# Optimization experiments

Hardware: AMD Instinct MI355X
Metric: run time of the kernel (lower is better)

## Reference

```python
import jax, jax.numpy as jnp
import numpy as np

N = 200000
W = 255  # hidden width hard-coded in the module


def _linear_params(key, fan_in, fan_out, w_std=0.02, b_val=0.0):
    kw, _ = jax.random.split(key)
    w = jax.random.normal(kw, (fan_in, fan_out), dtype=jnp.float32) * w_std
    b = jnp.full((fan_out,), b_val, dtype=jnp.float32)
    return w, b


def setup_inputs() -> dict:
    key = jax.random.key(0)
    ks = jax.random.split(key, 20)
    inp = {
        "opacity_emb": jax.random.normal(ks[0], (N, 1), dtype=jnp.float32),
        "shs_emb": jax.random.normal(ks[1], (N, 16, 3), dtype=jnp.float32),
        "time_emb": jax.random.uniform(ks[2], (N, 1), dtype=jnp.float32),
        "semantic_feature": jax.random.normal(ks[3], (N, 128), dtype=jnp.float32),
        "point": jax.random.normal(ks[4], (N, 3), dtype=jnp.float32),
        "scales_input": jax.random.normal(ks[5], (N, 3), dtype=jnp.float32),
        "rotations_input": jax.random.normal(ks[6], (N, 4), dtype=jnp.float32),
        "dx": jax.random.normal(ks[7], (N, 3), dtype=jnp.float32),
    }
    # mask_net: ReLU -> Linear(W,W) -> ReLU -> Linear(W,1) -> sigmoid
    inp["mask_w1"], inp["mask_b1"] = _linear_params(ks[8], W, W)
    inp["mask_w2"], inp["mask_b2"] = _linear_params(ks[9], W, 1)
    # deform heads: ReLU -> Linear(W,W) -> ReLU -> Linear(W,out)
    inp["pos_w1"], inp["pos_b1"] = _linear_params(ks[10], W, W)
    inp["pos_w2"], inp["pos_b2"] = _linear_params(ks[11], W, 3)
    inp["scl_w1"], inp["scl_b1"] = _linear_params(ks[12], W, W)
    inp["scl_w2"], inp["scl_b2"] = _linear_params(ks[13], W, 3)
    inp["rot_w1"], inp["rot_b1"] = _linear_params(ks[14], W, W)
    inp["rot_w2"], inp["rot_b2"] = _linear_params(ks[15], W, 4)
    inp["shs_w1"], inp["shs_b1"] = _linear_params(ks[16], W, W)
    inp["shs_w2"], inp["shs_b2"] = _linear_params(ks[17], W, 48)
    return inp


def _head(hidden, w1, b1, w2, b2):
    # ReLU -> Linear -> ReLU -> Linear (matches nn.Sequential in the module)
    h = jax.nn.relu(hidden)
    h = jax.nn.relu(h @ w1 + b1)
    return h @ w2 + b2


def _time_pos_enc(time_emb, n):
    # vectorized version of the scalar sin/cos for-loop: uses only time_emb[0, 0]
    t = time_emb[0, 0]
    i = jnp.arange(0, 64, 2, dtype=jnp.float32)          # even indices
    freq = jnp.power(jnp.float32(10000.0), i / jnp.float32(32.0))  # 10000**(2*i/64)
    enc = jnp.stack([jnp.sin(t / freq), jnp.cos(t / freq)], axis=1).reshape(64)
    return jnp.broadcast_to(enc[None, :], (n, 64))


def reference(opacity_emb, shs_emb, time_emb, semantic_feature, point,
              scales_input, rotations_input, dx,
              mask_w1, mask_b1, mask_w2, mask_b2,
              pos_w1, pos_b1, pos_w2, pos_b2,
              scl_w1, scl_b1, scl_w2, scl_b2,
              rot_w1, rot_b1, rot_w2, rot_b2,
              shs_w1, shs_b1, shs_w2, shs_b2):
    n = shs_emb.shape[0]
    shs_flat = shs_emb.reshape(n, 48)
    tpe = _time_pos_enc(time_emb, n)                     # [N, 64]
    hidden = jnp.concatenate(
        (point, rotations_input, scales_input, opacity_emb,
         shs_flat, semantic_feature, dx, time_emb, tpe), axis=1)  # [N, 255]

    mask = jax.nn.sigmoid(_head(hidden, mask_w1, mask_b1, mask_w2, mask_b2))  # [N, 1]

    dx_out = _head(hidden, pos_w1, pos_b1, pos_w2, pos_b2)        # [N, 3]
    pts = point + dx_out * mask

    ds = _head(hidden, scl_w1, scl_b1, scl_w2, scl_b2)            # [N, 3]
    scales = scales_input + ds * mask

    dr = _head(hidden, rot_w1, rot_b1, rot_w2, rot_b2)            # [N, 4]
    rotations = rotations_input + dr * mask

    opacity = opacity_emb[:, :1]

    dshs = _head(hidden, shs_w1, shs_b1, shs_w2, shs_b2).reshape(n, 16, 3)
    shs = shs_emb + dshs * mask[:, :, None]

    return (pts, scales, rotations, opacity, shs, dx_out, dshs)
```

## Files before the change

kernel.cpp:

```cpp
#include <hip/hip_runtime.h>
#include <math.h>

typedef unsigned short u16;
typedef __attribute__((ext_vector_type(8))) short short8;
typedef __attribute__((ext_vector_type(4))) float floatx4;

__device__ __forceinline__ u16 f2bf(float f) {
    union { float f; unsigned u; } v; v.f = f;
    unsigned r = v.u + 0x7fffu + ((v.u >> 16) & 1u);
    return (u16)(r >> 16);
}

struct WPtrs {
    const float* w1[5];
    const float* w2[5];
};

typedef const __attribute__((address_space(1))) unsigned GUA;
typedef __attribute__((address_space(3))) unsigned LUA;

__device__ __forceinline__ void stage32(const u16* gbase, u16* lbase, int wave, int lane) {
    const char* g = (const char*)gbase;
    char* l = (char*)lbase;
#pragma unroll
    for (int i = 0; i < 4; ++i) {
        int off = (wave * 4 + i) * 1024;
        __builtin_amdgcn_global_load_lds((GUA*)(g + off + lane * 16), (LUA*)(l + off), 16, 0, 0);
    }
}

__global__ void prep_weights(WPtrs p, const float* __restrict__ te,
                             u16* __restrict__ W1t, u16* __restrict__ W2t,
                             float* __restrict__ W2f, u16* __restrict__ enc)
{
    const int bid = blockIdx.x;
    const int tid = threadIdx.x;
    if (bid < 80) {
        __shared__ float tile[64 * 65];
        int h = bid / 16, t = bid % 16;
        int k0 = (t / 4) * 64, n0 = (t % 4) * 64;
        int nn = tid & 63, g = tid >> 6;
        const float* w1 = p.w1[h];
#pragma unroll
        for (int rep = 0; rep < 16; ++rep) {
            int kl = g * 16 + rep;
            int k = k0 + kl, nidx = n0 + nn;
            float v = (k < 255 && nidx < 255) ? w1[k * 255 + nidx] : 0.0f;
            tile[kl * 65 + nn] = v;
        }
        __syncthreads();
#pragma unroll
        for (int i = 0; i < 2; ++i) {
            int c = tid * 2 + i;
            int nl = c >> 3, kcl = c & 7;
            int n = n0 + nl;
            int kcg = (k0 >> 3) + kcl;
            short8 sv;
#pragma unroll
            for (int j = 0; j < 8; ++j)
                sv[j] = (short)f2bf(tile[(kcl * 8 + j) * 65 + nl]);
            *(short8*)(W1t + h * 65536 + n * 256 + (((kcg ^ (n & 31))) << 3)) = sv;
        }
    } else if (bid < 192) {
        int row = bid - 80;
        int h, roff, od;
        if (row < 16)      { h = 0; roff = 0;  od = 1; }
        else if (row < 32) { h = 1; roff = 16; od = 3; }
        else if (row < 48) { h = 2; roff = 32; od = 3; }
        else if (row < 64) { h = 3; roff = 48; od = 4; }
        else               { h = 4; roff = 64; od = 48; }
        int n2 = row - roff;
        int k = tid;
        float v = (k < 255 && n2 < od) ? p.w2[h][k * od + n2] : 0.0f;
        W2t[row * 256 + k] = f2bf(v);
        if (h < 4 && n2 < od) {
            int r11b = (h == 0) ? 0 : (h == 1) ? 1 : (h == 2) ? 4 : 7;
            W2f[(r11b + n2) * 256 + k] = v;
        }
    } else {
        if (tid < 64) {
            float t = te[0];
            float fi = (float)(tid & ~1);
            float freq = powf(10000.0f, fi * (1.0f / 32.0f));
            float a = t / freq;
            float v = (tid & 1) ? cosf(a) : sinf(a);
            enc[tid] = f2bf(fmaxf(v, 0.0f));
        }
    }
}

struct FusedArgs {
    const u16* W1t; const u16* W2t; const float* W2f; const u16* enc;
    const float* b1[5]; const float* b2[5];
    const float* opa; const float* shs; const float* te; const float* sem;
    const float* pt;  const float* scl; const float* rot; const float* dxp;
    float* out; int n;
};

__device__ __forceinline__ short8 gather8(const FusedArgs& A, int row, int c0)
{
    short8 sv;
    if (c0 >= 64 && c0 <= 176) {
        const float* s = A.sem + (size_t)row * 128 + (c0 - 59);
        float4 a = *(const float4*)(s);
        float4 b = *(const float4*)(s + 4);
        sv[0] = (short)f2bf(fmaxf(a.x, 0.f)); sv[1] = (short)f2bf(fmaxf(a.y, 0.f));
        sv[2] = (short)f2bf(fmaxf(a.z, 0.f)); sv[3] = (short)f2bf(fmaxf(a.w, 0.f));
        sv[4] = (short)f2bf(fmaxf(b.x, 0.f)); sv[5] = (short)f2bf(fmaxf(b.y, 0.f));
        sv[6] = (short)f2bf(fmaxf(b.z, 0.f)); sv[7] = (short)f2bf(fmaxf(b.w, 0.f));
    } else if (c0 >= 192) {
#pragma unroll
        for (int j = 0; j < 8; ++j) {
            int c = c0 + j;
            sv[j] = (c < 255) ? (short)A.enc[c - 191] : (short)0;
        }
    } else {
#pragma unroll
        for (int j = 0; j < 8; ++j) {
            int c = c0 + j;
            float v;
            if (c < 3)        v = A.pt[row * 3 + c];
            else if (c < 7)   v = A.rot[row * 4 + (c - 3)];
            else if (c < 10)  v = A.scl[row * 3 + (c - 7)];
            else if (c < 11)  v = A.opa[row];
            else if (c < 59)  v = A.shs[(size_t)row * 48 + (c - 11)];
            else if (c < 187) v = A.sem[(size_t)row * 128 + (c - 59)];
            else if (c < 190) v = A.dxp[row * 3 + (c - 187)];
            else if (c < 191) v = A.te[row];
            else { sv[j] = (short)A.enc[c - 191]; continue; }
            sv[j] = (short)f2bf(fmaxf(v, 0.0f));
        }
    }
    return sv;
}

__global__ __launch_bounds__(512, 4) void fused_all(FusedArgs A)
{
    __shared__ u16 W1L[2][16384];

    const int tid = threadIdx.x;
    const int wave = tid >> 6;
    const int lane = tid & 63;
    const int q = lane >> 4, ln = lane & 15;
    const int n = A.n;
    const size_t NN = (size_t)n;

    stage32(A.W1t, W1L[0], wave, lane);

    const int r0 = blockIdx.x * 128 + wave * 16;
    const int ra = min(r0 + ln, n - 1);
    const int grow = r0 + ln;

    short8 xf[8];
#pragma unroll
    for (int kk = 0; kk < 8; ++kk)
        xf[kk] = gather8(A, ra, kk * 32 + q * 8);

    __syncthreads();

    floatx4 acc[4];
    floatx4 acc2[3];
    float out2[4];
    float mkb = 0.f;

#pragma unroll 1
    for (int c = 0; c < 20; ++c) {
        const int h = c >> 2;
        const int Q = c & 3;
        if (c + 1 < 20)
            stage32(A.W1t + (size_t)(c + 1) * 16384, W1L[(c + 1) & 1], wave, lane);
        const u16* buf = W1L[c & 1];

#pragma unroll
        for (int ct = 0; ct < 4; ++ct) acc[ct] = (floatx4){0.f, 0.f, 0.f, 0.f};
#pragma unroll
        for (int kk = 0; kk < 8; ++kk) {
#pragma unroll
            for (int ct = 0; ct < 4; ++ct) {
                int nl = ct * 16 + ln;
                int sw = (kk * 4 + q) ^ (nl & 31);
                short8 wf = *(const short8*)(buf + nl * 256 + (sw << 3));
                acc[ct] = __builtin_amdgcn_mfma_f32_16x16x32_bf16(wf, xf[kk], acc[ct], 0, 0, 0);
            }
        }

        const float* b1h = A.b1[h];
#pragma unroll
        for (int ct = 0; ct < 4; ++ct) {
            floatx4 b4;
            if (Q == 3 && ct == 3) {
                if (q == 3) { b4.x = b1h[252]; b4.y = b1h[253]; b4.z = b1h[254]; b4.w = 0.f; }
                else        b4 = *(const floatx4*)(b1h + 240 + q * 4);
            } else {
                b4 = *(const floatx4*)(b1h + Q * 64 + ct * 16 + q * 4);
            }
            floatx4 v = acc[ct];
            v.x = fmaxf(v.x + b4.x, 0.f);
            v.y = fmaxf(v.y + b4.y, 0.f);
            v.z = fmaxf(v.z + b4.z, 0.f);
            v.w = fmaxf(v.w + b4.w, 0.f);
            acc[ct] = v;
        }

        if (h < 4) {
            const int od = (h == 0) ? 1 : (h == 3) ? 4 : 3;
            const int r11b = (h == 0) ? 0 : (h == 1) ? 1 : (h == 2) ? 4 : 7;
            if (Q == 0) {
#pragma unroll
                for (int m = 0; m < 4; ++m) out2[m] = 0.f;
            }
            const float* wb = A.W2f + r11b * 256 + Q * 64 + q * 4;
#pragma unroll
            for (int n2 = 0; n2 < 4; ++n2) {
                if (n2 < od) {
#pragma unroll
                    for (int ct = 0; ct < 4; ++ct) {
                        floatx4 w4 = *(const floatx4*)(wb + n2 * 256 + ct * 16);
                        out2[n2] = fmaf(acc[ct].x, w4.x, out2[n2]);
                        out2[n2] = fmaf(acc[ct].y, w4.y, out2[n2]);
                        out2[n2] = fmaf(acc[ct].z, w4.z, out2[n2]);
                        out2[n2] = fmaf(acc[ct].w, w4.w, out2[n2]);
                    }
                }
            }
            if (Q == 3) {
#pragma unroll
                for (int n2 = 0; n2 < 4; ++n2) {
                    float v = out2[n2];
                    v += __shfl_xor(v, 16, 64);
                    v += __shfl_xor(v, 32, 64);
                    out2[n2] = v;
                }
                const float* b2h = A.b2[h];
                if (h == 0) {
                    mkb = 1.0f / (1.0f + expf(-(out2[0] + b2h[0])));
                    if (q == 0 && grow < n) A.out[10 * NN + grow] = A.opa[grow];
                } else if (grow < n && q == 0) {
                    if (h == 1) {
#pragma unroll
                        for (int r = 0; r < 3; ++r) {
                            float raw = out2[r] + b2h[r];
                            A.out[59 * NN + (size_t)grow * 3 + r] = raw;
                            A.out[(size_t)grow * 3 + r] = A.pt[(size_t)grow * 3 + r] + raw * mkb;
                        }
                    } else if (h == 2) {
#pragma unroll
                        for (int r = 0; r < 3; ++r) {
                            float raw = out2[r] + b2h[r];
                            A.out[3 * NN + (size_t)grow * 3 + r] = A.scl[(size_t)grow * 3 + r] + raw * mkb;
                        }
                    } else {
#pragma unroll
                        for (int r = 0; r < 4; ++r) {
                            float raw = out2[r] + b2h[r];
                            A.out[6 * NN + (size_t)grow * 4 + r] = A.rot[(size_t)grow * 4 + r] + raw * mkb;
                        }
                    }
                }
            }
        } else {
            if (Q == 0) {
#pragma unroll
                for (int mt = 0; mt < 3; ++mt) acc2[mt] = (floatx4){0.f, 0.f, 0.f, 0.f};
            }
            const u16* w2th = A.W2t + 64 * 256;
#pragma unroll
            for (int ks = 0; ks < 2; ++ks) {
                int ksg = Q * 2 + ks;
                short8 a2[3];
#pragma unroll
                for (int mt = 0; mt < 3; ++mt)
                    a2[mt] = *(const short8*)(w2th + (mt * 16 + ln) * 256 + ksg * 32 + q * 8);
                short8 bfrag;
#pragma unroll
                for (int j = 0; j < 8; ++j) {
                    int idx = (((q * 2 + (j >> 2)) & 3) << 4) | ln;
                    float v0 = __shfl(acc[ks * 2 + 0][j & 3], idx, 64);
                    float v1 = __shfl(acc[ks * 2 + 1][j & 3], idx, 64);
                    bfrag[j] = (short)f2bf((q >> 1) ? v1 : v0);
                }
#pragma unroll
                for (int mt = 0; mt < 3; ++mt)
                    acc2[mt] = __builtin_amdgcn_mfma_f32_16x16x32_bf16(a2[mt], bfrag, acc2[mt], 0, 0, 0);
            }
            if (Q == 3 && grow < n) {
                const float* b2h = A.b2[4];
#pragma unroll
                for (int mt = 0; mt < 3; ++mt) {
                    int n2b = mt * 16 + q * 4;
                    floatx4 b2v = *(const floatx4*)(b2h + n2b);
                    floatx4 raw = acc2[mt] + b2v;
                    *(floatx4*)(A.out + 62 * NN + (size_t)grow * 48 + n2b) = raw;
                    floatx4 s = *(const floatx4*)(A.shs + (size_t)grow * 48 + n2b);
                    *(floatx4*)(A.out + 11 * NN + (size_t)grow * 48 + n2b) = s + raw * mkb;
                }
            }
        }

        __syncthreads();
    }
}

extern "C" void kernel_launch(void* const* d_in, const int* in_sizes, int n_in,
                              void* d_out, int out_size, void* d_ws, size_t ws_size,
                              hipStream_t stream)
{
    const float* opa  = (const float*)d_in[0];
    const float* shs  = (const float*)d_in[1];
    const float* te   = (const float*)d_in[2];
    const float* sem  = (const float*)d_in[3];
    const float* pt   = (const float*)d_in[4];
    const float* scl  = (const float*)d_in[5];
    const float* rot  = (const float*)d_in[6];
    const float* dx   = (const float*)d_in[7];

    WPtrs p;
    p.w1[0] = (const float*)d_in[8];  p.w2[0] = (const float*)d_in[10];
    p.w1[1] = (const float*)d_in[12]; p.w2[1] = (const float*)d_in[14];
    p.w1[2] = (const float*)d_in[16]; p.w2[2] = (const float*)d_in[18];
    p.w1[3] = (const float*)d_in[20]; p.w2[3] = (const float*)d_in[22];
    p.w1[4] = (const float*)d_in[24]; p.w2[4] = (const float*)d_in[26];

    const int n = in_sizes[0];

    char* ws = (char*)d_ws;
    u16*   W1t = (u16*)ws;
    u16*   W2t = W1t + 5 * 65536;
    float* W2f = (float*)(ws + 655360 + 57344);
    u16*   enc = (u16*)(ws + 655360 + 57344 + 11264);

    prep_weights<<<193, 256, 0, stream>>>(p, te, W1t, W2t, W2f, enc);

    FusedArgs A;
    A.W1t = W1t; A.W2t = W2t; A.W2f = W2f; A.enc = enc;
    A.b1[0] = (const float*)d_in[9];  A.b2[0] = (const float*)d_in[11];
    A.b1[1] = (const float*)d_in[13]; A.b2[1] = (const float*)d_in[15];
    A.b1[2] = (const float*)d_in[17]; A.b2[2] = (const float*)d_in[19];
    A.b1[3] = (const float*)d_in[21]; A.b2[3] = (const float*)d_in[23];
    A.b1[4] = (const float*)d_in[25]; A.b2[4] = (const float*)d_in[27];
    A.opa = opa; A.shs = shs; A.te = te; A.sem = sem;
    A.pt = pt; A.scl = scl; A.rot = rot; A.dxp = dx;
    A.out = (float*)d_out; A.n = n;

    int grid = (n + 127) / 128;
    fused_all<<<grid, 512, 0, stream>>>(A);
}
```

Before: 600.2 us.

## Fold constant time encoding into first-layer bias and double rows per wave

The 64 time-encoding columns are the same for every row, so their contribution W1[191:255]·enc is precomputed per head into an effective bias. This shrinks the first-layer K dimension from 256 to 192, which cuts the MFMA work and the LDS weight staging by a quarter. Each wave now handles 32 rows instead of 16 (256-thread blocks, launch bounds 256,3), so every LDS weight fragment feeds two MFMAs. In exchange the kernel holds twice the accumulators and input fragments per thread, which raises register pressure and may lower occupancy.

```diff
diff --git a/kernel.cpp b/kernel.cpp
--- a/kernel.cpp
+++ b/kernel.cpp
@@ -14,30 +14,31 @@
 struct WPtrs {
     const float* w1[5];
     const float* w2[5];
+    const float* b1[5];
 };
 
 typedef const __attribute__((address_space(1))) unsigned GUA;
 typedef __attribute__((address_space(3))) unsigned LUA;
 
-__device__ __forceinline__ void stage32(const u16* gbase, u16* lbase, int wave, int lane) {
+__device__ __forceinline__ void stage24(const u16* gbase, u16* lbase, int wave, int lane) {
     const char* g = (const char*)gbase;
     char* l = (char*)lbase;
 #pragma unroll
-    for (int i = 0; i < 4; ++i) {
-        int off = (wave * 4 + i) * 1024;
+    for (int i = 0; i < 6; ++i) {
+        int off = (wave * 6 + i) * 1024;
         __builtin_amdgcn_global_load_lds((GUA*)(g + off + lane * 16), (LUA*)(l + off), 16, 0, 0);
     }
 }
 
 __global__ void prep_weights(WPtrs p, const float* __restrict__ te,
                              u16* __restrict__ W1t, u16* __restrict__ W2t,
-                             float* __restrict__ W2f, u16* __restrict__ enc)
+                             float* __restrict__ W2f, float* __restrict__ b1eff)
 {
     const int bid = blockIdx.x;
     const int tid = threadIdx.x;
-    if (bid < 80) {
+    if (bid < 60) {
         __shared__ float tile[64 * 65];
-        int h = bid / 16, t = bid % 16;
+        int h = bid / 12, t = bid % 12;
         int k0 = (t / 4) * 64, n0 = (t % 4) * 64;
         int nn = tid & 63, g = tid >> 6;
         const float* w1 = p.w1[h];
@@ -45,7 +46,7 @@
         for (int rep = 0; rep < 16; ++rep) {
             int kl = g * 16 + rep;
             int k = k0 + kl, nidx = n0 + nn;
-            float v = (k < 255 && nidx < 255) ? w1[k * 255 + nidx] : 0.0f;
+            float v = (k < 191 && nidx < 255) ? w1[k * 255 + nidx] : 0.0f;
             tile[kl * 65 + nn] = v;
         }
         __syncthreads();
@@ -59,10 +60,10 @@
 #pragma unroll
             for (int j = 0; j < 8; ++j)
                 sv[j] = (short)f2bf(tile[(kcl * 8 + j) * 65 + nl]);
-            *(short8*)(W1t + h * 65536 + n * 256 + (((kcg ^ (n & 31))) << 3)) = sv;
-        }
-    } else if (bid < 192) {
-        int row = bid - 80;
+            *(short8*)(W1t + h * 49152 + n * 192 + ((kcg ^ (n & 7)) << 3)) = sv;
+        }
+    } else if (bid < 172) {
+        int row = bid - 60;
         int h, roff, od;
         if (row < 16)      { h = 0; roff = 0;  od = 1; }
         else if (row < 32) { h = 1; roff = 16; od = 3; }
@@ -78,20 +79,34 @@
             W2f[(r11b + n2) * 256 + k] = v;
         }
     } else {
+        __shared__ float encL[64];
         if (tid < 64) {
             float t = te[0];
             float fi = (float)(tid & ~1);
             float freq = powf(10000.0f, fi * (1.0f / 32.0f));
             float a = t / freq;
             float v = (tid & 1) ? cosf(a) : sinf(a);
-            enc[tid] = f2bf(fmaxf(v, 0.0f));
+            encL[tid] = fmaxf(v, 0.0f);
+        }
+        __syncthreads();
+        for (int e = tid; e < 5 * 256; e += 256) {
+            int h = e >> 8, col = e & 255;
+            float s = 0.0f;
+            if (col < 255) {
+                s = p.b1[h][col];
+                const float* w1 = p.w1[h];
+#pragma unroll 8
+                for (int j = 0; j < 64; ++j)
+                    s += w1[(191 + j) * 255 + col] * encL[j];
+            }
+            b1eff[h * 256 + col] = s;
         }
     }
 }
 
 struct FusedArgs {
-    const u16* W1t; const u16* W2t; const float* W2f; const u16* enc;
-    const float* b1[5]; const float* b2[5];
+    const u16* W1t; const u16* W2t; const float* W2f; const float* b1eff;
+    const float* b2[5];
     const float* opa; const float* shs; const float* te; const float* sem;
     const float* pt;  const float* scl; const float* rot; const float* dxp;
     float* out; int n;
@@ -108,12 +123,6 @@
         sv[2] = (short)f2bf(fmaxf(a.z, 0.f)); sv[3] = (short)f2bf(fmaxf(a.w, 0.f));
         sv[4] = (short)f2bf(fmaxf(b.x, 0.f)); sv[5] = (short)f2bf(fmaxf(b.y, 0.f));
         sv[6] = (short)f2bf(fmaxf(b.z, 0.f)); sv[7] = (short)f2bf(fmaxf(b.w, 0.f));
-    } else if (c0 >= 192) {
-#pragma unroll
-        for (int j = 0; j < 8; ++j) {
-            int c = c0 + j;
-            sv[j] = (c < 255) ? (short)A.enc[c - 191] : (short)0;
-        }
     } else {
 #pragma unroll
         for (int j = 0; j < 8; ++j) {
@@ -127,16 +136,16 @@
             else if (c < 187) v = A.sem[(size_t)row * 128 + (c - 59)];
             else if (c < 190) v = A.dxp[row * 3 + (c - 187)];
             else if (c < 191) v = A.te[row];
-            else { sv[j] = (short)A.enc[c - 191]; continue; }
+            else              v = 0.0f;
             sv[j] = (short)f2bf(fmaxf(v, 0.0f));
         }
     }
     return sv;
 }
 
-__global__ __launch_bounds__(512, 4) void fused_all(FusedArgs A)
+__global__ __launch_bounds__(256, 3) void fused_all(FusedArgs A)
 {
-    __shared__ u16 W1L[2][16384];
+    __shared__ u16 W1L[2][12288];
 
     const int tid = threadIdx.x;
     const int wave = tid >> 6;
@@ -145,61 +154,65 @@
     const int n = A.n;
     const size_t NN = (size_t)n;
 
-    stage32(A.W1t, W1L[0], wave, lane);
-
-    const int r0 = blockIdx.x * 128 + wave * 16;
-    const int ra = min(r0 + ln, n - 1);
-    const int grow = r0 + ln;
-
-    short8 xf[8];
-#pragma unroll
-    for (int kk = 0; kk < 8; ++kk)
-        xf[kk] = gather8(A, ra, kk * 32 + q * 8);
+    stage24(A.W1t, W1L[0], wave, lane);
+
+    const int r0 = blockIdx.x * 128 + wave * 32;
+    const int ra0 = min(r0 + ln, n - 1);
+    const int ra1 = min(r0 + 16 + ln, n - 1);
+    const int g0 = r0 + ln, g1 = r0 + 16 + ln;
+
+    short8 xf[2][6];
+#pragma unroll
+    for (int kk = 0; kk < 6; ++kk) {
+        int c0 = kk * 32 + q * 8;
+        xf[0][kk] = gather8(A, ra0, c0);
+        xf[1][kk] = gather8(A, ra1, c0);
+    }
 
     __syncthreads();
 
-    floatx4 acc[4];
-    floatx4 acc2[3];
-    float out2[4];
-    float mkb = 0.f;
+    floatx4 acc[4][2];
+    floatx4 acc2[3][2];
+    float out2[4][2];
+    float mkb0 = 0.f, mkb1 = 0.f;
 
 #pragma unroll 1
     for (int c = 0; c < 20; ++c) {
         const int h = c >> 2;
         const int Q = c & 3;
         if (c + 1 < 20)
-            stage32(A.W1t + (size_t)(c + 1) * 16384, W1L[(c + 1) & 1], wave, lane);
+            stage24(A.W1t + (c + 1) * 12288, W1L[(c + 1) & 1], wave, lane);
         const u16* buf = W1L[c & 1];
 
 #pragma unroll
-        for (int ct = 0; ct < 4; ++ct) acc[ct] = (floatx4){0.f, 0.f, 0.f, 0.f};
-#pragma unroll
-        for (int kk = 0; kk < 8; ++kk) {
+        for (int ct = 0; ct < 4; ++ct) {
+            acc[ct][0] = (floatx4){0.f, 0.f, 0.f, 0.f};
+            acc[ct][1] = (floatx4){0.f, 0.f, 0.f, 0.f};
+        }
+#pragma unroll
+        for (int kk = 0; kk < 6; ++kk) {
 #pragma unroll
             for (int ct = 0; ct < 4; ++ct) {
                 int nl = ct * 16 + ln;
-                int sw = (kk * 4 + q) ^ (nl & 31);
-                short8 wf = *(const short8*)(buf + nl * 256 + (sw << 3));
-                acc[ct] = __builtin_amdgcn_mfma_f32_16x16x32_bf16(wf, xf[kk], acc[ct], 0, 0, 0);
-            }
-        }
-
-        const float* b1h = A.b1[h];
+                int sw = (kk * 4 + q) ^ (ln & 7);
+                short8 wf = *(const short8*)(buf + nl * 192 + (sw << 3));
+                acc[ct][0] = __builtin_amdgcn_mfma_f32_16x16x32_bf16(wf, xf[0][kk], acc[ct][0], 0, 0, 0);
+                acc[ct][1] = __builtin_amdgcn_mfma_f32_16x16x32_bf16(wf, xf[1][kk], acc[ct][1], 0, 0, 0);
+            }
+        }
+
 #pragma unroll
         for (int ct = 0; ct < 4; ++ct) {
-            floatx4 b4;
-            if (Q == 3 && ct == 3) {
-                if (q == 3) { b4.x = b1h[252]; b4.y = b1h[253]; b4.z = b1h[254]; b4.w = 0.f; }
-                else        b4 = *(const floatx4*)(b1h + 240 + q * 4);
-            } else {
-                b4 = *(const floatx4*)(b1h + Q * 64 + ct * 16 + q * 4);
-            }
-            floatx4 v = acc[ct];
-            v.x = fmaxf(v.x + b4.x, 0.f);
-            v.y = fmaxf(v.y + b4.y, 0.f);
-            v.z = fmaxf(v.z + b4.z, 0.f);
-            v.w = fmaxf(v.w + b4.w, 0.f);
-            acc[ct] = v;
+            floatx4 b4 = *(const floatx4*)(A.b1eff + h * 256 + Q * 64 + ct * 16 + q * 4);
+#pragma unroll
+            for (int t = 0; t < 2; ++t) {
+                floatx4 v = acc[ct][t];
+                v.x = fmaxf(v.x + b4.x, 0.f);
+                v.y = fmaxf(v.y + b4.y, 0.f);
+                v.z = fmaxf(v.z + b4.z, 0.f);
+                v.w = fmaxf(v.w + b4.w, 0.f);
+                acc[ct][t] = v;
+            }
         }
 
         if (h < 4) {
@@ -207,7 +220,7 @@
             const int r11b = (h == 0) ? 0 : (h == 1) ? 1 : (h == 2) ? 4 : 7;
             if (Q == 0) {
 #pragma unroll
-                for (int m = 0; m < 4; ++m) out2[m] = 0.f;
+                for (int m = 0; m < 4; ++m) { out2[m][0] = 0.f; out2[m][1] = 0.f; }
             }
             const float* wb = A.W2f + r11b * 256 + Q * 64 + q * 4;
 #pragma unroll
@@ -216,44 +229,61 @@
 #pragma unroll
                     for (int ct = 0; ct < 4; ++ct) {
                         floatx4 w4 = *(const floatx4*)(wb + n2 * 256 + ct * 16);
-                        out2[n2] = fmaf(acc[ct].x, w4.x, out2[n2]);
-                        out2[n2] = fmaf(acc[ct].y, w4.y, out2[n2]);
-                        out2[n2] = fmaf(acc[ct].z, w4.z, out2[n2]);
-                        out2[n2] = fmaf(acc[ct].w, w4.w, out2[n2]);
+#pragma unroll
+                        for (int t = 0; t < 2; ++t) {
+                            out2[n2][t] = fmaf(acc[ct][t].x, w4.x, out2[n2][t]);
+                            out2[n2][t] = fmaf(acc[ct][t].y, w4.y, out2[n2][t]);
+                            out2[n2][t] = fmaf(acc[ct][t].z, w4.z, out2[n2][t]);
+                            out2[n2][t] = fmaf(acc[ct][t].w, w4.w, out2[n2][t]);
+                        }
                     }
                 }
             }
             if (Q == 3) {
 #pragma unroll
                 for (int n2 = 0; n2 < 4; ++n2) {
-                    float v = out2[n2];
-                    v += __shfl_xor(v, 16, 64);
-                    v += __shfl_xor(v, 32, 64);
-                    out2[n2] = v;
+#pragma unroll
+                    for (int t = 0; t < 2; ++t) {
+                        float v = out2[n2][t];
+                        v += __shfl_xor(v, 16, 64);
+                        v += __shfl_xor(v, 32, 64);
+                        out2[n2][t] = v;
+                    }
                 }
                 const float* b2h = A.b2[h];
                 if (h == 0) {
-                    mkb = 1.0f / (1.0f + expf(-(out2[0] + b2h[0])));
-                    if (q == 0 && grow < n) A.out[10 * NN + grow] = A.opa[grow];
-                } else if (grow < n && q == 0) {
-                    if (h == 1) {
-#pragma unroll
-                        for (int r = 0; r < 3; ++r) {
-                            float raw = out2[r] + b2h[r];
-                            A.out[59 * NN + (size_t)grow * 3 + r] = raw;
-                            A.out[(size_t)grow * 3 + r] = A.pt[(size_t)grow * 3 + r] + raw * mkb;
-                        }
-                    } else if (h == 2) {
-#pragma unroll
-                        for (int r = 0; r < 3; ++r) {
-                            float raw = out2[r] + b2h[r];
-                            A.out[3 * NN + (size_t)grow * 3 + r] = A.scl[(size_t)grow * 3 + r] + raw * mkb;
-                        }
-                    } else {
-#pragma unroll
-                        for (int r = 0; r < 4; ++r) {
-                            float raw = out2[r] + b2h[r];
-                            A.out[6 * NN + (size_t)grow * 4 + r] = A.rot[(size_t)grow * 4 + r] + raw * mkb;
+                    mkb0 = 1.0f / (1.0f + expf(-(out2[0][0] + b2h[0])));
+                    mkb1 = 1.0f / (1.0f + expf(-(out2[0][1] + b2h[0])));
+                    if (q == 0) {
+                        if (g0 < n) A.out[10 * NN + g0] = A.opa[g0];
+                        if (g1 < n) A.out[10 * NN + g1] = A.opa[g1];
+                    }
+                } else if (q == 0) {
+#pragma unroll
+                    for (int t = 0; t < 2; ++t) {
+                        int grow = t ? g1 : g0;
+                        float mk = t ? mkb1 : mkb0;
+                        if (grow < n) {
+                            if (h == 1) {
+#pragma unroll
+                                for (int r = 0; r < 3; ++r) {
+                                    float raw = out2[r][t] + b2h[r];
+                                    A.out[59 * NN + (size_t)grow * 3 + r] = raw;
+                                    A.out[(size_t)grow * 3 + r] = A.pt[(size_t)grow * 3 + r] + raw * mk;
+                                }
+                            } else if (h == 2) {
+#pragma unroll
+                                for (int r = 0; r < 3; ++r) {
+                                    float raw = out2[r][t] + b2h[r];
+                                    A.out[3 * NN + (size_t)grow * 3 + r] = A.scl[(size_t)grow * 3 + r] + raw * mk;
+                                }
+                            } else {
+#pragma unroll
+                                for (int r = 0; r < 4; ++r) {
+                                    float raw = out2[r][t] + b2h[r];
+                                    A.out[6 * NN + (size_t)grow * 4 + r] = A.rot[(size_t)grow * 4 + r] + raw * mk;
+                                }
+                            }
                         }
                     }
                 }
@@ -261,7 +291,10 @@
         } else {
             if (Q == 0) {
 #pragma unroll
-                for (int mt = 0; mt < 3; ++mt) acc2[mt] = (floatx4){0.f, 0.f, 0.f, 0.f};
+                for (int mt = 0; mt < 3; ++mt) {
+                    acc2[mt][0] = (floatx4){0.f, 0.f, 0.f, 0.f};
+                    acc2[mt][1] = (floatx4){0.f, 0.f, 0.f, 0.f};
+                }
             }
             const u16* w2th = A.W2t + 64 * 256;
 #pragma unroll
@@ -271,28 +304,38 @@
 #pragma unroll
                 for (int mt = 0; mt < 3; ++mt)
                     a2[mt] = *(const short8*)(w2th + (mt * 16 + ln) * 256 + ksg * 32 + q * 8);
-                short8 bfrag;
-#pragma unroll
-                for (int j = 0; j < 8; ++j) {
-                    int idx = (((q * 2 + (j >> 2)) & 3) << 4) | ln;
-                    float v0 = __shfl(acc[ks * 2 + 0][j & 3], idx, 64);
-                    float v1 = __shfl(acc[ks * 2 + 1][j & 3], idx, 64);
-                    bfrag[j] = (short)f2bf((q >> 1) ? v1 : v0);
-                }
-#pragma unroll
-                for (int mt = 0; mt < 3; ++mt)
-                    acc2[mt] = __builtin_amdgcn_mfma_f32_16x16x32_bf16(a2[mt], bfrag, acc2[mt], 0, 0, 0);
-            }
-            if (Q == 3 && grow < n) {
+#pragma unroll
+                for (int t = 0; t < 2; ++t) {
+                    short8 bfrag;
+#pragma unroll
+                    for (int j = 0; j < 8; ++j) {
+                        int idx = (((q * 2 + (j >> 2)) & 3) << 4) | ln;
+                        float v0 = __shfl(acc[ks * 2 + 0][t][j & 3], idx, 64);
+                        float v1 = __shfl(acc[ks * 2 + 1][t][j & 3], idx, 64);
+                        bfrag[j] = (short)f2bf((q >> 1) ? v1 : v0);
+                    }
+#pragma unroll
+                    for (int mt = 0; mt < 3; ++mt)
+                        acc2[mt][t] = __builtin_amdgcn_mfma_f32_16x16x32_bf16(a2[mt], bfrag, acc2[mt][t], 0, 0, 0);
+                }
+            }
+            if (Q == 3) {
                 const float* b2h = A.b2[4];
 #pragma unroll
-                for (int mt = 0; mt < 3; ++mt) {
-                    int n2b = mt * 16 + q * 4;
-                    floatx4 b2v = *(const floatx4*)(b2h + n2b);
-                    floatx4 raw = acc2[mt] + b2v;
-                    *(floatx4*)(A.out + 62 * NN + (size_t)grow * 48 + n2b) = raw;
-                    floatx4 s = *(const floatx4*)(A.shs + (size_t)grow * 48 + n2b);
-                    *(floatx4*)(A.out + 11 * NN + (size_t)grow * 48 + n2b) = s + raw * mkb;
+                for (int t = 0; t < 2; ++t) {
+                    int grow = t ? g1 : g0;
+                    float mk = t ? mkb1 : mkb0;
+                    if (grow < n) {
+#pragma unroll
+                        for (int mt = 0; mt < 3; ++mt) {
+                            int n2b = mt * 16 + q * 4;
+                            floatx4 b2v = *(const floatx4*)(b2h + n2b);
+                            floatx4 raw = acc2[mt][t] + b2v;
+                            *(floatx4*)(A.out + 62 * NN + (size_t)grow * 48 + n2b) = raw;
+                            floatx4 s = *(const floatx4*)(A.shs + (size_t)grow * 48 + n2b);
+                            *(floatx4*)(A.out + 11 * NN + (size_t)grow * 48 + n2b) = s + raw * mk;
+                        }
+                    }
                 }
             }
         }
@@ -315,33 +358,33 @@
     const float* dx   = (const float*)d_in[7];
 
     WPtrs p;
-    p.w1[0] = (const float*)d_in[8];  p.w2[0] = (const float*)d_in[10];
-    p.w1[1] = (const float*)d_in[12]; p.w2[1] = (const float*)d_in[14];
-    p.w1[2] = (const float*)d_in[16]; p.w2[2] = (const float*)d_in[18];
-    p.w1[3] = (const float*)d_in[20]; p.w2[3] = (const float*)d_in[22];
-    p.w1[4] = (const float*)d_in[24]; p.w2[4] = (const float*)d_in[26];
+    p.w1[0] = (const float*)d_in[8];  p.w2[0] = (const float*)d_in[10]; p.b1[0] = (const float*)d_in[9];
+    p.w1[1] = (const float*)d_in[12]; p.w2[1] = (const float*)d_in[14]; p.b1[1] = (const float*)d_in[13];
+    p.w1[2] = (const float*)d_in[16]; p.w2[2] = (const float*)d_in[18]; p.b1[2] = (const float*)d_in[17];
+    p.w1[3] = (const float*)d_in[20]; p.w2[3] = (const float*)d_in[22]; p.b1[3] = (const float*)d_in[21];
+    p.w1[4] = (const float*)d_in[24]; p.w2[4] = (const float*)d_in[26]; p.b1[4] = (const float*)d_in[25];
 
     const int n = in_sizes[0];
 
     char* ws = (char*)d_ws;
-    u16*   W1t = (u16*)ws;
-    u16*   W2t = W1t + 5 * 65536;
-    float* W2f = (float*)(ws + 655360 + 57344);
-    u16*   enc = (u16*)(ws + 655360 + 57344 + 11264);
-
-    prep_weights<<<193, 256, 0, stream>>>(p, te, W1t, W2t, W2f, enc);
+    u16*   W1t   = (u16*)ws;
+    u16*   W2t   = (u16*)(ws + 491520);
+    float* W2f   = (float*)(ws + 491520 + 57344);
+    float* b1eff = (float*)(ws + 491520 + 57344 + 11264);
+
+    prep_weights<<<173, 256, 0, stream>>>(p, te, W1t, W2t, W2f, b1eff);
 
     FusedArgs A;
-    A.W1t = W1t; A.W2t = W2t; A.W2f = W2f; A.enc = enc;
-    A.b1[0] = (const float*)d_in[9];  A.b2[0] = (const float*)d_in[11];
-    A.b1[1] = (const float*)d_in[13]; A.b2[1] = (const float*)d_in[15];
-    A.b1[2] = (const float*)d_in[17]; A.b2[2] = (const float*)d_in[19];
-    A.b1[3] = (const float*)d_in[21]; A.b2[3] = (const float*)d_in[23];
-    A.b1[4] = (const float*)d_in[25]; A.b2[4] = (const float*)d_in[27];
+    A.W1t = W1t; A.W2t = W2t; A.W2f = W2f; A.b1eff = b1eff;
+    A.b2[0] = (const float*)d_in[11];
+    A.b2[1] = (const float*)d_in[15];
+    A.b2[2] = (const float*)d_in[19];
+    A.b2[3] = (const float*)d_in[23];
+    A.b2[4] = (const float*)d_in[27];
     A.opa = opa; A.shs = shs; A.te = te; A.sem = sem;
     A.pt = pt; A.scl = scl; A.rot = rot; A.dxp = dx;
     A.out = (float*)d_out; A.n = n;
 
     int grid = (n + 127) / 128;
-    fused_all<<<grid, 512, 0, stream>>>(A);
-}
+    fused_all<<<grid, 256, 0, stream>>>(A);
+}
```

New measurement: 534.4 us. -11.0%, faster.
